# Optimization experiments

Measured on AMD Instinct MI355X. Metric: run time of the kernel, lower is better.

Reference implementation:

```python
import jax, jax.numpy as jnp
import numpy as np

B, H, S, D = 2, 16, 2048, 64


def setup_inputs() -> dict:
    key = jax.random.key(0)
    kq, kk, kv = jax.random.split(key, 3)
    query = jax.random.normal(kq, (B, H, S, D), dtype=jnp.float32)
    k_ = jax.random.normal(kk, (B, H, S, D), dtype=jnp.float32)
    value = jax.random.normal(kv, (B, H, S, D), dtype=jnp.float32)
    # causal mask, broadcastable to (B, H, S, S); 0 => masked out
    mask = jnp.tril(jnp.ones((S, S), dtype=jnp.int32))[None, None, :, :]
    return {"query": query, "key": k_, "value": value, "mask": mask}


def reference(query, key, value, mask):
    dim = key.shape[-1]
    # scores: [b, h, s_q, s_k]
    scores = jnp.einsum('bhqe,bhke->bhqk', query, key) * (dim ** -0.5)
    scores = jnp.where(mask == 0, -jnp.inf, scores)
    attention = jax.nn.softmax(scores, axis=-1)
    output = jnp.einsum('bhqk,bhkd->bhqd', attention, value)
    return output, attention
```

## Files before the change

kernel.cpp:

```cpp
#include <hip/hip_runtime.h>

#define S_LEN 2048
#define DHEAD 64
#define NQT   32
#define BH    32
#define SCALE_LOG2E 0.18033688011112042f

typedef __bf16 bf16_t;
typedef bf16_t bf16x8 __attribute__((ext_vector_type(8)));
typedef bf16_t bf16x4 __attribute__((ext_vector_type(4)));
typedef float  f32x4  __attribute__((ext_vector_type(4)));

static __device__ __forceinline__ f32x4 mfma16(bf16x8 a, bf16x8 b, f32x4 c) {
    return __builtin_amdgcn_mfma_f32_16x16x32_bf16(a, b, c, 0, 0, 0);
}

static __device__ __forceinline__ int sw(int row, int colByte) {
    return (row << 7) + (colByte ^ ((row & 7) << 4));
}

template <bool SCALE>
static __device__ __forceinline__ void stage_tile(const float* __restrict__ src,
                                                  char* dst, int tid) {
#pragma unroll
    for (int i = 0; i < 2; ++i) {
        int f = tid + (i << 8);
        int r = f >> 3;
        int c = (f & 7) << 3;
        const f32x4* sp = (const f32x4*)(src + r * 64 + c);
        f32x4 a = sp[0], b = sp[1];
        if (SCALE) { a = a * SCALE_LOG2E; b = b * SCALE_LOG2E; }
        bf16x8 v;
        v[0] = (bf16_t)a[0]; v[1] = (bf16_t)a[1]; v[2] = (bf16_t)a[2]; v[3] = (bf16_t)a[3];
        v[4] = (bf16_t)b[0]; v[5] = (bf16_t)b[1]; v[6] = (bf16_t)b[2]; v[7] = (bf16_t)b[3];
        *(bf16x8*)(dst + sw(r, c << 1)) = v;
    }
}

static __device__ __forceinline__ void stage_vt(const float* __restrict__ src,
                                                char* dst, int tid) {
    int k0 = (tid >> 4) << 2;
    int d0 = (tid & 15) << 2;
    f32x4 r0 = *(const f32x4*)(src + (k0 + 0) * 64 + d0);
    f32x4 r1 = *(const f32x4*)(src + (k0 + 1) * 64 + d0);
    f32x4 r2 = *(const f32x4*)(src + (k0 + 2) * 64 + d0);
    f32x4 r3 = *(const f32x4*)(src + (k0 + 3) * 64 + d0);
#pragma unroll
    for (int j = 0; j < 4; ++j) {
        int d = d0 + j;
        bf16x4 w;
        w[0] = (bf16_t)r0[j]; w[1] = (bf16_t)r1[j];
        w[2] = (bf16_t)r2[j]; w[3] = (bf16_t)r3[j];
        *(bf16x4*)(dst + (d << 7) + ((k0 << 1) ^ ((d & 7) << 4))) = w;
    }
}

extern "C" __global__ void __launch_bounds__(256)
attn_flash(const float* __restrict__ Q, const float* __restrict__ K,
           const float* __restrict__ V, float* __restrict__ out,
           float* __restrict__ mrow, float* __restrict__ ilrow) {
    __shared__ __align__(16) char QsB[8192];
    __shared__ __align__(16) char KsB[8192];
    __shared__ __align__(16) char VtB[8192];
    __shared__ __align__(16) char PsB[4][2048];

    const int tid  = threadIdx.x;
    const int bid  = blockIdx.x;
    const int bh   = bid & 31;
    const int qt   = 31 - (bid >> 5);
    const int lane = tid & 63;
    const int wq   = tid >> 6;
    const int g    = lane >> 4;
    const int qc   = lane & 15;

    const size_t hoff = (size_t)bh * (S_LEN * DHEAD);
    const float* Qb = Q + hoff;
    const float* Kb = K + hoff;
    const float* Vb = V + hoff;
    float* outb = out + hoff;

    const int q0 = qt << 6;

    stage_tile<true>(Qb + q0 * DHEAD, QsB, tid);
    __syncthreads();

    const int qrow = (wq << 4) + qc;
    const int qg   = q0 + qrow;
    bf16x8 bq0 = *(const bf16x8*)(QsB + sw(qrow, (g << 4)));
    bf16x8 bq1 = *(const bf16x8*)(QsB + sw(qrow, 64 + (g << 4)));

    float m = -1e30f, l = 0.f;
    f32x4 oacc[4];
#pragma unroll
    for (int i = 0; i < 4; ++i) oacc[i] = (f32x4){0.f, 0.f, 0.f, 0.f};

    char* PsW = PsB[wq];

    for (int kt = 0; kt <= qt; ++kt) {
        __syncthreads();
        stage_tile<false>(Kb + kt * 4096, KsB, tid);
        stage_vt(Vb + kt * 4096, VtB, tid);
        __syncthreads();

        float sv[16];
#pragma unroll
        for (int kb = 0; kb < 4; ++kb) {
            const int ar = (kb << 4) + qc;
            bf16x8 a0 = *(const bf16x8*)(KsB + sw(ar, (g << 4)));
            bf16x8 a1 = *(const bf16x8*)(KsB + sw(ar, 64 + (g << 4)));
            f32x4 acc = {0.f, 0.f, 0.f, 0.f};
            acc = mfma16(a0, bq0, acc);
            acc = mfma16(a1, bq1, acc);
#pragma unroll
            for (int r = 0; r < 4; ++r) sv[(kb << 2) + r] = acc[r];
        }
        if (kt == qt) {
#pragma unroll
            for (int kb = 0; kb < 4; ++kb)
#pragma unroll
                for (int r = 0; r < 4; ++r) {
                    int kg = (kt << 6) + (kb << 4) + (g << 2) + r;
                    if (kg > qg) sv[(kb << 2) + r] = -1e30f;
                }
        }
        float mx = sv[0];
#pragma unroll
        for (int i = 1; i < 16; ++i) mx = fmaxf(mx, sv[i]);
        mx = fmaxf(mx, __shfl_xor(mx, 16));
        mx = fmaxf(mx, __shfl_xor(mx, 32));
        const float mn   = fmaxf(m, mx);
        const float corr = exp2f(m - mn);

        float p[16], se = 0.f;
#pragma unroll
        for (int i = 0; i < 16; ++i) { p[i] = exp2f(sv[i] - mn); se += p[i]; }
        se += __shfl_xor(se, 16);
        se += __shfl_xor(se, 32);
        l = l * corr + se;
        m = mn;
#pragma unroll
        for (int i = 0; i < 4; ++i) oacc[i] = oacc[i] * corr;

#pragma unroll
        for (int kb = 0; kb < 4; ++kb) {
            bf16x4 pb;
            pb[0] = (bf16_t)p[(kb << 2) + 0]; pb[1] = (bf16_t)p[(kb << 2) + 1];
            pb[2] = (bf16_t)p[(kb << 2) + 2]; pb[3] = (bf16_t)p[(kb << 2) + 3];
            *(bf16x4*)(PsW + (qc << 7) + (((kb << 5) + (g << 3)) ^ ((qc & 7) << 4))) = pb;
        }
        bf16x8 bp0 = *(const bf16x8*)(PsW + sw(qc, (g << 4)));
        bf16x8 bp1 = *(const bf16x8*)(PsW + sw(qc, 64 + (g << 4)));
#pragma unroll
        for (int dc = 0; dc < 4; ++dc) {
            const int vr = (dc << 4) + qc;
            bf16x8 av0 = *(const bf16x8*)(VtB + sw(vr, (g << 4)));
            bf16x8 av1 = *(const bf16x8*)(VtB + sw(vr, 64 + (g << 4)));
            oacc[dc] = mfma16(av0, bp0, oacc[dc]);
            oacc[dc] = mfma16(av1, bp1, oacc[dc]);
        }
    }

    const float il = 1.0f / l;
#pragma unroll
    for (int dc = 0; dc < 4; ++dc) {
        f32x4 o = oacc[dc] * il;
        *(f32x4*)(outb + (size_t)qg * DHEAD + (dc << 4) + (g << 2)) = o;
    }
    if (g == 0) {
        mrow [bh * S_LEN + qg] = m;
        ilrow[bh * S_LEN + qg] = il;
    }
}

extern "C" __global__ void __launch_bounds__(256)
attn_probs(const float* __restrict__ Q, const float* __restrict__ K,
           const float* __restrict__ mrow, const float* __restrict__ ilrow,
           float* __restrict__ att) {
    const int tid = threadIdx.x;
    const int bid = blockIdx.x;
    const int bh  = bid >> 10;
    const int qt  = (bid >> 5) & 31;
    const int kt  = bid & 31;

    float* attb = att + (size_t)bh * ((size_t)S_LEN * S_LEN);
    const int q0 = qt << 6;
    const int k0 = kt << 6;

    if (kt > qt) {
        f32x4 z = {0.f, 0.f, 0.f, 0.f};
#pragma unroll
        for (int i = 0; i < 4; ++i) {
            int f = tid + (i << 8);
            int r = f >> 4;
            int c = (f & 15) << 2;
            __builtin_nontemporal_store(z, (f32x4*)(attb + (size_t)(q0 + r) * S_LEN + k0 + c));
        }
        return;
    }

    __shared__ __align__(16) char QsB[8192];
    __shared__ __align__(16) char KsB[8192];

    const size_t hoff = (size_t)bh * (S_LEN * DHEAD);
    stage_tile<true >(Q + hoff + q0 * DHEAD, QsB, tid);
    stage_tile<false>(K + hoff + k0 * DHEAD, KsB, tid);
    __syncthreads();

    const int lane = tid & 63;
    const int wq   = tid >> 6;
    const int g    = lane >> 4;
    const int qc   = lane & 15;
    const int qrow = (wq << 4) + qc;
    const int qg   = q0 + qrow;

    bf16x8 bq0 = *(const bf16x8*)(QsB + sw(qrow, (g << 4)));
    bf16x8 bq1 = *(const bf16x8*)(QsB + sw(qrow, 64 + (g << 4)));

    const float m  = mrow [bh * S_LEN + qg];
    const float il = ilrow[bh * S_LEN + qg];

#pragma unroll
    for (int kb = 0; kb < 4; ++kb) {
        const int ar = (kb << 4) + qc;
        bf16x8 a0 = *(const bf16x8*)(KsB + sw(ar, (g << 4)));
        bf16x8 a1 = *(const bf16x8*)(KsB + sw(ar, 64 + (g << 4)));
        f32x4 acc = {0.f, 0.f, 0.f, 0.f};
        acc = mfma16(a0, bq0, acc);
        acc = mfma16(a1, bq1, acc);
        f32x4 pw;
#pragma unroll
        for (int r = 0; r < 4; ++r) {
            int kg = k0 + (kb << 4) + (g << 2) + r;
            float p = exp2f(acc[r] - m) * il;
            pw[r] = (kt == qt && kg > qg) ? 0.f : p;
        }
        __builtin_nontemporal_store(
            pw, (f32x4*)(attb + (size_t)qg * S_LEN + k0 + (kb << 4) + (g << 2)));
    }
}

extern "C" void kernel_launch(void* const* d_in, const int* in_sizes, int n_in,
                              void* d_out, int out_size, void* d_ws, size_t ws_size,
                              hipStream_t stream) {
    const float* Q = (const float*)d_in[0];
    const float* K = (const float*)d_in[1];
    const float* V = (const float*)d_in[2];
    float* out = (float*)d_out;
    float* att = out + (size_t)BH * S_LEN * DHEAD;
    float* mrow  = (float*)d_ws;
    float* ilrow = mrow + (size_t)BH * S_LEN;

    hipLaunchKernelGGL(attn_flash, dim3(BH * NQT), dim3(256), 0, stream,
                       Q, K, V, out, mrow, ilrow);
    hipLaunchKernelGGL(attn_probs, dim3(BH * NQT * NQT), dim3(256), 0, stream,
                       Q, K, mrow, ilrow, att);
}
```

Baseline: 677.7 us.

## Prefetch K/V tiles into registers and coalesce probability stores via LDS

In the flash kernel, the next K and V tiles are loaded from global memory into registers while the current tile is being computed. They are then converted to bf16 and written to shared memory at the top of the next iteration, which hides global load latency at the cost of more registers. In the probs kernel, each probability tile is written to a swizzled LDS buffer and then stored to global memory as full contiguous 64-float rows. This replaces the scattered 16-byte-per-lane stores and should improve write coalescing for the large attention-matrix output, at the cost of 16KB of extra LDS and one more barrier.

```diff
diff --git a/kernel.cpp b/kernel.cpp
--- a/kernel.cpp
+++ b/kernel.cpp
@@ -37,24 +37,6 @@
     }
 }
 
-static __device__ __forceinline__ void stage_vt(const float* __restrict__ src,
-                                                char* dst, int tid) {
-    int k0 = (tid >> 4) << 2;
-    int d0 = (tid & 15) << 2;
-    f32x4 r0 = *(const f32x4*)(src + (k0 + 0) * 64 + d0);
-    f32x4 r1 = *(const f32x4*)(src + (k0 + 1) * 64 + d0);
-    f32x4 r2 = *(const f32x4*)(src + (k0 + 2) * 64 + d0);
-    f32x4 r3 = *(const f32x4*)(src + (k0 + 3) * 64 + d0);
-#pragma unroll
-    for (int j = 0; j < 4; ++j) {
-        int d = d0 + j;
-        bf16x4 w;
-        w[0] = (bf16_t)r0[j]; w[1] = (bf16_t)r1[j];
-        w[2] = (bf16_t)r2[j]; w[3] = (bf16_t)r3[j];
-        *(bf16x4*)(dst + (d << 7) + ((k0 << 1) ^ ((d & 7) << 4))) = w;
-    }
-}
-
 extern "C" __global__ void __launch_bounds__(256)
 attn_flash(const float* __restrict__ Q, const float* __restrict__ K,
            const float* __restrict__ V, float* __restrict__ out,
@@ -96,11 +78,48 @@
 
     char* PsW = PsB[wq];
 
+    const int kr_r  = tid >> 3;
+    const int kr_c  = (tid & 7) << 3;
+    const int vk0   = (tid >> 4) << 2;
+    const int vd0   = (tid & 15) << 2;
+    f32x4 kr0a, kr0b, kr1a, kr1b, vr0, vr1, vr2, vr3;
+
+#define LOAD_TILE_REGS(kt_)                                                   \
+    {                                                                         \
+        const float* ks_ = Kb + (kt_) * 4096;                                 \
+        kr0a = *(const f32x4*)(ks_ + kr_r * 64 + kr_c);                       \
+        kr0b = *(const f32x4*)(ks_ + kr_r * 64 + kr_c + 4);                   \
+        kr1a = *(const f32x4*)(ks_ + (kr_r + 32) * 64 + kr_c);                \
+        kr1b = *(const f32x4*)(ks_ + (kr_r + 32) * 64 + kr_c + 4);            \
+        const float* vs_ = Vb + (kt_) * 4096;                                 \
+        vr0 = *(const f32x4*)(vs_ + (vk0 + 0) * 64 + vd0);                    \
+        vr1 = *(const f32x4*)(vs_ + (vk0 + 1) * 64 + vd0);                    \
+        vr2 = *(const f32x4*)(vs_ + (vk0 + 2) * 64 + vd0);                    \
+        vr3 = *(const f32x4*)(vs_ + (vk0 + 3) * 64 + vd0);                    \
+    }
+
+    LOAD_TILE_REGS(0)
+
     for (int kt = 0; kt <= qt; ++kt) {
+        {
+            bf16x8 v;
+            v[0] = (bf16_t)kr0a[0]; v[1] = (bf16_t)kr0a[1]; v[2] = (bf16_t)kr0a[2]; v[3] = (bf16_t)kr0a[3];
+            v[4] = (bf16_t)kr0b[0]; v[5] = (bf16_t)kr0b[1]; v[6] = (bf16_t)kr0b[2]; v[7] = (bf16_t)kr0b[3];
+            *(bf16x8*)(KsB + sw(kr_r, kr_c << 1)) = v;
+            v[0] = (bf16_t)kr1a[0]; v[1] = (bf16_t)kr1a[1]; v[2] = (bf16_t)kr1a[2]; v[3] = (bf16_t)kr1a[3];
+            v[4] = (bf16_t)kr1b[0]; v[5] = (bf16_t)kr1b[1]; v[6] = (bf16_t)kr1b[2]; v[7] = (bf16_t)kr1b[3];
+            *(bf16x8*)(KsB + sw(kr_r + 32, kr_c << 1)) = v;
+#pragma unroll
+            for (int j = 0; j < 4; ++j) {
+                int d = vd0 + j;
+                bf16x4 w;
+                w[0] = (bf16_t)vr0[j]; w[1] = (bf16_t)vr1[j];
+                w[2] = (bf16_t)vr2[j]; w[3] = (bf16_t)vr3[j];
+                *(bf16x4*)(VtB + (d << 7) + ((vk0 << 1) ^ ((d & 7) << 4))) = w;
+            }
+        }
         __syncthreads();
-        stage_tile<false>(Kb + kt * 4096, KsB, tid);
-        stage_vt(Vb + kt * 4096, VtB, tid);
-        __syncthreads();
+        if (kt < qt) LOAD_TILE_REGS(kt + 1)
 
         float sv[16];
 #pragma unroll
@@ -158,6 +177,7 @@
             oacc[dc] = mfma16(av0, bp0, oacc[dc]);
             oacc[dc] = mfma16(av1, bp1, oacc[dc]);
         }
+        __syncthreads();
     }
 
     const float il = 1.0f / l;
@@ -200,6 +220,7 @@
 
     __shared__ __align__(16) char QsB[8192];
     __shared__ __align__(16) char KsB[8192];
+    __shared__ __align__(16) float Pt[4096];
 
     const size_t hoff = (size_t)bh * (S_LEN * DHEAD);
     stage_tile<true >(Q + hoff + q0 * DHEAD, QsB, tid);
@@ -234,8 +255,18 @@
             float p = exp2f(acc[r] - m) * il;
             pw[r] = (kt == qt && kg > qg) ? 0.f : p;
         }
+        int colf = (kb << 4) + (g << 2);
+        *(f32x4*)&Pt[(qrow << 6) + (colf ^ ((qrow & 7) << 2))] = pw;
+    }
+    __syncthreads();
+
+#pragma unroll
+    for (int i = 0; i < 4; ++i) {
+        int row  = (i << 4) + (tid >> 4);
+        int colf = (tid & 15) << 2;
+        f32x4 v = *(const f32x4*)&Pt[(row << 6) + (colf ^ ((row & 7) << 2))];
         __builtin_nontemporal_store(
-            pw, (f32x4*)(attb + (size_t)qg * S_LEN + k0 + (kb << 4) + (g << 2)));
+            v, (f32x4*)(attb + (size_t)(q0 + row) * S_LEN + k0 + colf));
     }
 }
 
```

Result: faster. 623.0 us (-8.1%).
